# Kernel optimization log

Hardware: AMD Instinct MI355X
Metric: run time of the kernel (lower is better)

## Reference

```python
import jax, jax.numpy as jnp
import numpy as np

NUM_EXPERTS = 8
EMBED_DIM = 512
NUM_LAYERS = 2
LN_EPS = 1e-5


def _all_pairs_hyperedges(E):
    # static 'all_pairs' strategy: one hyperedge per unordered expert pair
    nodes, edges = [], []
    eid = 0
    for i in range(E):
        for j in range(i + 1, E):
            nodes += [i, j]
            edges += [eid, eid]
            eid += 1
    return np.asarray(nodes, np.int32), np.asarray(edges, np.int32)


def setup_inputs() -> dict:
    key = jax.random.key(0)
    ks = jax.random.split(key, 4)
    B, L, E, D = 8, 1024, NUM_EXPERTS, EMBED_DIM
    nodes, edges = _all_pairs_hyperedges(E)
    return {
        "expert_outputs": jax.random.normal(ks[0], (B, L, E, D), jnp.float32),
        # HypergraphConv: lin has bias=False, conv bias is separate
        "hgnn_w": jax.random.normal(ks[1], (NUM_LAYERS, D, D), jnp.float32) * 0.02,
        "hgnn_b": jnp.zeros((NUM_LAYERS, D), jnp.float32),
        # combiner: Linear(D,D) -> GELU -> LayerNorm(D)
        "comb_w": jax.random.normal(ks[2], (D, D), jnp.float32) * 0.02,
        "comb_b": jnp.zeros((D,), jnp.float32),
        "ln_gamma": jnp.ones((D,), jnp.float32),
        "ln_beta": jnp.zeros((D,), jnp.float32),
        "nodes_idx": jnp.asarray(nodes),
        "edges_idx": jnp.asarray(edges),
    }


def _hypergraph_conv(h, W, b, nodes_idx, edges_idx, num_edges, d_inv, b_inv):
    # h: [N, E, D] with N = B*L token-graphs sharing the static hyperedge structure.
    # PyG HypergraphConv (no attention, unit edge weights):
    #   out = D^{-1} H B^{-1} H^T (h @ W^T) + b
    x = jnp.einsum('ned,fd->nef', h, W)  # lin(x), bias=False
    N, E, D = x.shape
    # node -> hyperedge scatter-add, scaled by inverse hyperedge degree B^{-1}
    m = jnp.zeros((N, num_edges, D), x.dtype)
    m = m.at[:, edges_idx].add(x[:, nodes_idx]) * b_inv[None, :, None]
    # hyperedge -> node scatter-add, scaled by inverse node degree D^{-1}
    out = jnp.zeros((N, E, D), x.dtype)
    out = out.at[:, nodes_idx].add(m[:, edges_idx]) * d_inv[None, :, None]
    return out + b


def reference(expert_outputs, hgnn_w, hgnn_b, comb_w, comb_b, ln_gamma, ln_beta, nodes_idx, edges_idx):
    B, L, E, D = expert_outputs.shape
    num_edges = nodes_idx.shape[0] // 2  # all_pairs: exactly 2 nodes per hyperedge
    # degree normalizations (unit hyperedge weights)
    deg = jnp.zeros((E,), expert_outputs.dtype).at[nodes_idx].add(1.0)
    d_inv = jnp.where(deg > 0, 1.0 / deg, 0.0)
    edeg = jnp.zeros((num_edges,), expert_outputs.dtype).at[edges_idx].add(1.0)
    b_inv = jnp.where(edeg > 0, 1.0 / edeg, 0.0)

    h = expert_outputs.reshape(B * L, E, D)
    for l in range(hgnn_w.shape[0]):
        h = _hypergraph_conv(h, hgnn_w[l], hgnn_b[l], nodes_idx, edges_idx, num_edges, d_inv, b_inv)

    pooled = h.reshape(B, L, E, D).mean(axis=2)  # [B, L, D]
    z = jax.nn.gelu(pooled @ comb_w.T + comb_b, approximate=False)  # torch nn.GELU = exact
    mu = jnp.mean(z, axis=-1, keepdims=True)
    var = jnp.var(z, axis=-1, keepdims=True)
    return (z - mu) / jnp.sqrt(var + LN_EPS) * ln_gamma + ln_beta
```

## Files before the change

kernel.cpp:

```cpp
#include <hip/hip_runtime.h>
#include <hip/hip_bf16.h>
#include <math.h>


#define DD 512
#define NTOK 8192

typedef short s16x8 __attribute__((ext_vector_type(8)));
typedef short s16x4 __attribute__((ext_vector_type(4)));
typedef float f32x4 __attribute__((ext_vector_type(4)));

static __device__ __forceinline__ short f2bf(float x) {
  unsigned u = __builtin_bit_cast(unsigned, x);
  unsigned r = (u + 0x7fffu + ((u >> 16) & 1u)) >> 16;
  return (short)r;
}

__global__ __launch_bounds__(256) void pool_kernel(const float* __restrict__ in,
                                                   short* __restrict__ gbf) {
  const int total = NTOK * (DD / 4);
  for (int i = blockIdx.x * blockDim.x + threadIdx.x; i < total;
       i += gridDim.x * blockDim.x) {
    int n = i >> 7;
    int d4 = (i & 127) << 2;
    const float* p = in + (size_t)n * (8 * DD) + d4;
    f32x4 s = {0.f, 0.f, 0.f, 0.f};
#pragma unroll
    for (int e = 0; e < 8; ++e) s += *(const f32x4*)(p + e * DD);
    s *= 0.125f;
    s16x4 o;
    o[0] = f2bf(s[0]); o[1] = f2bf(s[1]); o[2] = f2bf(s[2]); o[3] = f2bf(s[3]);
    *(s16x4*)(gbf + (size_t)n * DD + d4) = o;
  }
}

__global__ __launch_bounds__(256) void cast2_kernel(const float* __restrict__ w2,
                                                    const float* __restrict__ wc,
                                                    short* __restrict__ w2b,
                                                    short* __restrict__ wcb) {
  int i = blockIdx.x * blockDim.x + threadIdx.x;
  const float* src = (i < 65536) ? w2 : wc;
  short* dst = (i < 65536) ? w2b : wcb;
  int j = (i & 65535) << 2;
  f32x4 v = *(const f32x4*)(src + j);
  s16x4 o;
  o[0] = f2bf(v[0]); o[1] = f2bf(v[1]); o[2] = f2bf(v[2]); o[3] = f2bf(v[3]);
  *(s16x4*)(dst + j) = o;
}

__global__ __launch_bounds__(256) void casttr_kernel(const float* __restrict__ w1,
                                                     short* __restrict__ w1t) {
  __shared__ float t[32][33];
  int bx = blockIdx.x & 15, by = blockIdx.x >> 4;
  int tx = threadIdx.x & 31, ty8 = threadIdx.x >> 5;
  int r0 = by * 32, c0 = bx * 32;
#pragma unroll
  for (int j = 0; j < 4; ++j) {
    int r = ty8 * 4 + j;
    t[r][tx] = w1[(size_t)(r0 + r) * DD + c0 + tx];
  }
  __syncthreads();
#pragma unroll
  for (int j = 0; j < 4; ++j) {
    int r = ty8 * 4 + j;
    w1t[(size_t)(c0 + r) * DD + r0 + tx] = f2bf(t[tx][r]);
  }
}

__global__ __launch_bounds__(256) void mv_kernel(const float* __restrict__ M,
                                                 const float* __restrict__ v,
                                                 const float* __restrict__ add,
                                                 float* __restrict__ outv) {
  int w = (blockIdx.x * blockDim.x + threadIdx.x) >> 6;
  int l = threadIdx.x & 63;
  if (w >= DD) return;
  float s = 0.f;
  for (int k = l; k < DD; k += 64) s += M[(size_t)w * DD + k] * v[k];
#pragma unroll
  for (int m = 32; m; m >>= 1) s += __shfl_xor(s, m);
  if (l == 0) outv[w] = s + add[w];
}

__global__ __launch_bounds__(256) void wgemm_kernel(const short* __restrict__ A,
                                                    const short* __restrict__ B,
                                                    short* __restrict__ Out) {
  int w = threadIdx.x >> 6, l = threadIdx.x & 63;
  int lr = l & 15, lg = l >> 4;
  int m0 = (blockIdx.x >> 3) * 64 + w * 16;
  int n0 = (blockIdx.x & 7) * 64;
  f32x4 acc[4] = {};
  const short* ap = A + (size_t)(m0 + lr) * DD + 8 * lg;
  const short* bp = B + (size_t)(n0 + lr) * DD + 8 * lg;
#pragma unroll
  for (int k0 = 0; k0 < DD; k0 += 32) {
    s16x8 a = *(const s16x8*)(ap + k0);
#pragma unroll
    for (int f = 0; f < 4; ++f) {
      s16x8 b = *(const s16x8*)(bp + (size_t)f * 16 * DD + k0);
      acc[f] = __builtin_amdgcn_mfma_f32_16x16x32_bf16(a, b, acc[f], 0, 0, 0);
    }
  }
#pragma unroll
  for (int f = 0; f < 4; ++f)
#pragma unroll
    for (int r = 0; r < 4; ++r)
      Out[(size_t)(m0 + lg * 4 + r) * DD + n0 + f * 16 + lr] = f2bf(acc[f][r]);
}

__global__ __launch_bounds__(256) void main_kernel(
    const short* __restrict__ gbf, const short* __restrict__ wcomb,
    const float* __restrict__ cbias, const float* __restrict__ gamma,
    const float* __restrict__ beta, float* __restrict__ out) {
  __shared__ short As[32 * DD];
  __shared__ float red[32][4][2];
  int tid = threadIdx.x;
  int w = tid >> 6, l = tid & 63;
  int lr = l & 15, lg = l >> 4;
  int m0 = blockIdx.x * 32;

  {
    const char* gs = (const char*)(gbf + (size_t)m0 * DD);
    char* ls = (char*)As;
#pragma unroll
    for (int j = 0; j < 8; ++j) {
      int ci = tid + 256 * j;
      int row = ci >> 6;
      int bo = (ci & 63) << 4;
      s16x8 v = *(const s16x8*)(gs + row * 1024 + bo);
      *(s16x8*)(ls + row * 1024 + (bo ^ ((row & 7) << 4))) = v;
    }
  }
  __syncthreads();

  f32x4 acc[2][8] = {};
  const short* bbase = wcomb + (size_t)(w * 128 + lr) * DD + 8 * lg;
  const char* lsc = (const char*)As;
  for (int k0 = 0; k0 < DD; k0 += 32) {
    int kb = (k0 + 8 * lg) * 2;
    int row0 = lr, row1 = 16 + lr;
    s16x8 a0 = *(const s16x8*)(lsc + row0 * 1024 + (kb ^ ((row0 & 7) << 4)));
    s16x8 a1 = *(const s16x8*)(lsc + row1 * 1024 + (kb ^ ((row1 & 7) << 4)));
#pragma unroll
    for (int f = 0; f < 8; ++f) {
      s16x8 b = *(const s16x8*)(bbase + (size_t)f * 16 * DD + k0);
      acc[0][f] = __builtin_amdgcn_mfma_f32_16x16x32_bf16(a0, b, acc[0][f], 0, 0, 0);
      acc[1][f] = __builtin_amdgcn_mfma_f32_16x16x32_bf16(a1, b, acc[1][f], 0, 0, 0);
    }
  }

  int cbase = w * 128 + lr;
  float s1[2][4] = {}, s2[2][4] = {};
#pragma unroll
  for (int mi = 0; mi < 2; ++mi)
#pragma unroll
    for (int f = 0; f < 8; ++f) {
      float cb = cbias[cbase + f * 16];
#pragma unroll
      for (int r = 0; r < 4; ++r) {
        float x = acc[mi][f][r] + cb;
        float z = 0.5f * x * (1.0f + erff(x * 0.70710678118f));
        acc[mi][f][r] = z;
        s1[mi][r] += z;
        s2[mi][r] += z * z;
      }
    }
#pragma unroll
  for (int m = 1; m < 16; m <<= 1)
#pragma unroll
    for (int mi = 0; mi < 2; ++mi)
#pragma unroll
      for (int r = 0; r < 4; ++r) {
        s1[mi][r] += __shfl_xor(s1[mi][r], m);
        s2[mi][r] += __shfl_xor(s2[mi][r], m);
      }
  if (lr == 0) {
#pragma unroll
    for (int mi = 0; mi < 2; ++mi)
#pragma unroll
      for (int r = 0; r < 4; ++r) {
        int row = mi * 16 + lg * 4 + r;
        red[row][w][0] = s1[mi][r];
        red[row][w][1] = s2[mi][r];
      }
  }
  __syncthreads();
#pragma unroll
  for (int mi = 0; mi < 2; ++mi)
#pragma unroll
    for (int r = 0; r < 4; ++r) {
      int row = mi * 16 + lg * 4 + r;
      float t1 = red[row][0][0] + red[row][1][0] + red[row][2][0] + red[row][3][0];
      float t2 = red[row][0][1] + red[row][1][1] + red[row][2][1] + red[row][3][1];
      float mu = t1 * (1.0f / 512.0f);
      float var = t2 * (1.0f / 512.0f) - mu * mu;
      float rs = rsqrtf(var + 1e-5f);
      float* op = out + (size_t)(m0 + row) * DD;
#pragma unroll
      for (int f = 0; f < 8; ++f) {
        int c = cbase + f * 16;
        op[c] = (acc[mi][f][r] - mu) * rs * gamma[c] + beta[c];
      }
    }
}

extern "C" void kernel_launch(void* const* d_in, const int* in_sizes, int n_in,
                              void* d_out, int out_size, void* d_ws, size_t ws_size,
                              hipStream_t stream) {
  const float* x   = (const float*)d_in[0];
  const float* hw  = (const float*)d_in[1];
  const float* hb  = (const float*)d_in[2];
  const float* cw  = (const float*)d_in[3];
  const float* cb  = (const float*)d_in[4];
  const float* gam = (const float*)d_in[5];
  const float* bet = (const float*)d_in[6];
  float* out = (float*)d_out;

  char* ws = (char*)d_ws;
  short* gbf   = (short*)ws; ws += (size_t)NTOK * DD * 2;
  short* w1t   = (short*)ws; ws += DD * DD * 2;
  short* w2b   = (short*)ws; ws += DD * DD * 2;
  short* wcb   = (short*)ws; ws += DD * DD * 2;
  short* w21t  = (short*)ws; ws += DD * DD * 2;
  short* wcomb = (short*)ws; ws += DD * DD * 2;
  float* tmpv  = (float*)ws; ws += DD * 4;
  float* cbias = (float*)ws; ws += DD * 4;

  const float* W1 = hw;
  const float* W2 = hw + DD * DD;
  const float* b1 = hb;
  const float* b2 = hb + DD;

  pool_kernel<<<2048, 256, 0, stream>>>(x, gbf);
  casttr_kernel<<<256, 256, 0, stream>>>(W1, w1t);
  cast2_kernel<<<512, 256, 0, stream>>>(W2, cw, w2b, wcb);
  mv_kernel<<<128, 256, 0, stream>>>(W2, b1, b2, tmpv);
  mv_kernel<<<128, 256, 0, stream>>>(cw, tmpv, cb, cbias);
  wgemm_kernel<<<64, 256, 0, stream>>>(w1t, w2b, w21t);
  wgemm_kernel<<<64, 256, 0, stream>>>(wcb, w21t, wcomb);
  main_kernel<<<NTOK / 32, 256, 0, stream>>>(gbf, wcomb, cbias, gam, bet, out);
}
```

Before: 280.1 us.

## Fuse pooling into main GEMM kernel and merge weight-prep launches

```diff
diff --git a/kernel.cpp b/kernel.cpp
--- a/kernel.cpp
+++ b/kernel.cpp
@@ -16,63 +16,21 @@
   return (short)r;
 }
 
-__global__ __launch_bounds__(256) void pool_kernel(const float* __restrict__ in,
-                                                   short* __restrict__ gbf) {
-  const int total = NTOK * (DD / 4);
-  for (int i = blockIdx.x * blockDim.x + threadIdx.x; i < total;
-       i += gridDim.x * blockDim.x) {
-    int n = i >> 7;
-    int d4 = (i & 127) << 2;
-    const float* p = in + (size_t)n * (8 * DD) + d4;
-    f32x4 s = {0.f, 0.f, 0.f, 0.f};
-#pragma unroll
-    for (int e = 0; e < 8; ++e) s += *(const f32x4*)(p + e * DD);
-    s *= 0.125f;
-    s16x4 o;
-    o[0] = f2bf(s[0]); o[1] = f2bf(s[1]); o[2] = f2bf(s[2]); o[3] = f2bf(s[3]);
-    *(s16x4*)(gbf + (size_t)n * DD + d4) = o;
-  }
-}
-
-__global__ __launch_bounds__(256) void cast2_kernel(const float* __restrict__ w2,
-                                                    const float* __restrict__ wc,
-                                                    short* __restrict__ w2b,
-                                                    short* __restrict__ wcb) {
-  int i = blockIdx.x * blockDim.x + threadIdx.x;
-  const float* src = (i < 65536) ? w2 : wc;
-  short* dst = (i < 65536) ? w2b : wcb;
-  int j = (i & 65535) << 2;
+static __device__ __forceinline__ void do_cast4(const float* __restrict__ src,
+                                                short* __restrict__ dst, int i) {
+  int j = i << 2;
   f32x4 v = *(const f32x4*)(src + j);
   s16x4 o;
   o[0] = f2bf(v[0]); o[1] = f2bf(v[1]); o[2] = f2bf(v[2]); o[3] = f2bf(v[3]);
   *(s16x4*)(dst + j) = o;
 }
 
-__global__ __launch_bounds__(256) void casttr_kernel(const float* __restrict__ w1,
-                                                     short* __restrict__ w1t) {
-  __shared__ float t[32][33];
-  int bx = blockIdx.x & 15, by = blockIdx.x >> 4;
-  int tx = threadIdx.x & 31, ty8 = threadIdx.x >> 5;
-  int r0 = by * 32, c0 = bx * 32;
-#pragma unroll
-  for (int j = 0; j < 4; ++j) {
-    int r = ty8 * 4 + j;
-    t[r][tx] = w1[(size_t)(r0 + r) * DD + c0 + tx];
-  }
-  __syncthreads();
-#pragma unroll
-  for (int j = 0; j < 4; ++j) {
-    int r = ty8 * 4 + j;
-    w1t[(size_t)(c0 + r) * DD + r0 + tx] = f2bf(t[tx][r]);
-  }
-}
-
-__global__ __launch_bounds__(256) void mv_kernel(const float* __restrict__ M,
-                                                 const float* __restrict__ v,
-                                                 const float* __restrict__ add,
-                                                 float* __restrict__ outv) {
-  int w = (blockIdx.x * blockDim.x + threadIdx.x) >> 6;
-  int l = threadIdx.x & 63;
+static __device__ __forceinline__ void do_mv(const float* __restrict__ M,
+                                             const float* __restrict__ v,
+                                             const float* __restrict__ add,
+                                             float* __restrict__ outv,
+                                             int gtid) {
+  int w = gtid >> 6, l = gtid & 63;
   if (w >= DD) return;
   float s = 0.f;
   for (int k = l; k < DD; k += 64) s += M[(size_t)w * DD + k] * v[k];
@@ -81,13 +39,46 @@
   if (l == 0) outv[w] = s + add[w];
 }
 
-__global__ __launch_bounds__(256) void wgemm_kernel(const short* __restrict__ A,
-                                                    const short* __restrict__ B,
-                                                    short* __restrict__ Out) {
-  int w = threadIdx.x >> 6, l = threadIdx.x & 63;
+__global__ __launch_bounds__(256) void prep1_kernel(
+    const float* __restrict__ w1, const float* __restrict__ w2,
+    const float* __restrict__ wc, const float* __restrict__ b1,
+    const float* __restrict__ b2, short* __restrict__ w1t,
+    short* __restrict__ w2b, short* __restrict__ wcb,
+    float* __restrict__ tmpv) {
+  int b = blockIdx.x, tid = threadIdx.x;
+  if (b < 256) {
+    __shared__ float t[32][33];
+    int bx = b & 15, by = b >> 4;
+    int tx = tid & 31, ty8 = tid >> 5;
+    int r0 = by * 32, c0 = bx * 32;
+#pragma unroll
+    for (int j = 0; j < 4; ++j) {
+      int r = ty8 * 4 + j;
+      t[r][tx] = w1[(size_t)(r0 + r) * DD + c0 + tx];
+    }
+    __syncthreads();
+#pragma unroll
+    for (int j = 0; j < 4; ++j) {
+      int r = ty8 * 4 + j;
+      w1t[(size_t)(c0 + r) * DD + r0 + tx] = f2bf(t[tx][r]);
+    }
+  } else if (b < 768) {
+    int i = (b - 256) * 256 + tid;
+    if (i < 65536) do_cast4(w2, w2b, i);
+    else           do_cast4(wc, wcb, i - 65536);
+  } else {
+    do_mv(w2, b1, b2, tmpv, (b - 768) * 256 + tid);
+  }
+}
+
+static __device__ __forceinline__ void do_wgemm(const short* __restrict__ A,
+                                                const short* __restrict__ B,
+                                                short* __restrict__ Out,
+                                                int b, int tid) {
+  int w = tid >> 6, l = tid & 63;
   int lr = l & 15, lg = l >> 4;
-  int m0 = (blockIdx.x >> 3) * 64 + w * 16;
-  int n0 = (blockIdx.x & 7) * 64;
+  int m0 = (b >> 3) * 64 + w * 16;
+  int n0 = (b & 7) * 64;
   f32x4 acc[4] = {};
   const short* ap = A + (size_t)(m0 + lr) * DD + 8 * lg;
   const short* bp = B + (size_t)(n0 + lr) * DD + 8 * lg;
@@ -96,8 +87,8 @@
     s16x8 a = *(const s16x8*)(ap + k0);
 #pragma unroll
     for (int f = 0; f < 4; ++f) {
-      s16x8 b = *(const s16x8*)(bp + (size_t)f * 16 * DD + k0);
-      acc[f] = __builtin_amdgcn_mfma_f32_16x16x32_bf16(a, b, acc[f], 0, 0, 0);
+      s16x8 bb = *(const s16x8*)(bp + (size_t)f * 16 * DD + k0);
+      acc[f] = __builtin_amdgcn_mfma_f32_16x16x32_bf16(a, bb, acc[f], 0, 0, 0);
     }
   }
 #pragma unroll
@@ -107,100 +98,112 @@
       Out[(size_t)(m0 + lg * 4 + r) * DD + n0 + f * 16 + lr] = f2bf(acc[f][r]);
 }
 
+__global__ __launch_bounds__(256) void prep2_kernel(
+    const short* __restrict__ w1t, const short* __restrict__ w2b,
+    short* __restrict__ w21t, const float* __restrict__ wc,
+    const float* __restrict__ tmpv, const float* __restrict__ cb,
+    float* __restrict__ cbias) {
+  int b = blockIdx.x, tid = threadIdx.x;
+  if (b < 64) do_wgemm(w1t, w2b, w21t, b, tid);
+  else        do_mv(wc, tmpv, cb, cbias, (b - 64) * 256 + tid);
+}
+
+__global__ __launch_bounds__(256) void prep3_kernel(const short* __restrict__ wcb,
+                                                    const short* __restrict__ w21t,
+                                                    short* __restrict__ wcomb) {
+  do_wgemm(wcb, w21t, wcomb, blockIdx.x, threadIdx.x);
+}
+
 __global__ __launch_bounds__(256) void main_kernel(
-    const short* __restrict__ gbf, const short* __restrict__ wcomb,
+    const float* __restrict__ x, const short* __restrict__ wcomb,
     const float* __restrict__ cbias, const float* __restrict__ gamma,
     const float* __restrict__ beta, float* __restrict__ out) {
-  __shared__ short As[32 * DD];
-  __shared__ float red[32][4][2];
+  __shared__ short As[16 * DD];
+  __shared__ float red[16][4][2];
   int tid = threadIdx.x;
   int w = tid >> 6, l = tid & 63;
   int lr = l & 15, lg = l >> 4;
-  int m0 = blockIdx.x * 32;
+  int m0 = blockIdx.x * 16;
 
   {
-    const char* gs = (const char*)(gbf + (size_t)m0 * DD);
+    const float* xb = x + (size_t)m0 * (8 * DD);
     char* ls = (char*)As;
 #pragma unroll
     for (int j = 0; j < 8; ++j) {
-      int ci = tid + 256 * j;
-      int row = ci >> 6;
-      int bo = (ci & 63) << 4;
-      s16x8 v = *(const s16x8*)(gs + row * 1024 + bo);
-      *(s16x8*)(ls + row * 1024 + (bo ^ ((row & 7) << 4))) = v;
+      int i = tid + 256 * j;
+      int n = i >> 7;
+      int d4 = (i & 127) << 2;
+      const float* p = xb + n * (8 * DD) + d4;
+      f32x4 s = {0.f, 0.f, 0.f, 0.f};
+#pragma unroll
+      for (int e = 0; e < 8; ++e) s += *(const f32x4*)(p + e * DD);
+      s *= 0.125f;
+      s16x4 o;
+      o[0] = f2bf(s[0]); o[1] = f2bf(s[1]); o[2] = f2bf(s[2]); o[3] = f2bf(s[3]);
+      int bo = d4 << 1;
+      *(s16x4*)(ls + n * 1024 + (bo ^ ((n & 7) << 4))) = o;
     }
   }
   __syncthreads();
 
-  f32x4 acc[2][8] = {};
+  f32x4 acc[8] = {};
   const short* bbase = wcomb + (size_t)(w * 128 + lr) * DD + 8 * lg;
   const char* lsc = (const char*)As;
   for (int k0 = 0; k0 < DD; k0 += 32) {
     int kb = (k0 + 8 * lg) * 2;
-    int row0 = lr, row1 = 16 + lr;
-    s16x8 a0 = *(const s16x8*)(lsc + row0 * 1024 + (kb ^ ((row0 & 7) << 4)));
-    s16x8 a1 = *(const s16x8*)(lsc + row1 * 1024 + (kb ^ ((row1 & 7) << 4)));
+    s16x8 a = *(const s16x8*)(lsc + lr * 1024 + (kb ^ ((lr & 7) << 4)));
 #pragma unroll
     for (int f = 0; f < 8; ++f) {
       s16x8 b = *(const s16x8*)(bbase + (size_t)f * 16 * DD + k0);
-      acc[0][f] = __builtin_amdgcn_mfma_f32_16x16x32_bf16(a0, b, acc[0][f], 0, 0, 0);
-      acc[1][f] = __builtin_amdgcn_mfma_f32_16x16x32_bf16(a1, b, acc[1][f], 0, 0, 0);
+      acc[f] = __builtin_amdgcn_mfma_f32_16x16x32_bf16(a, b, acc[f], 0, 0, 0);
     }
   }
 
   int cbase = w * 128 + lr;
-  float s1[2][4] = {}, s2[2][4] = {};
-#pragma unroll
-  for (int mi = 0; mi < 2; ++mi)
+  float s1[4] = {}, s2[4] = {};
+#pragma unroll
+  for (int f = 0; f < 8; ++f) {
+    float cb = cbias[cbase + f * 16];
+#pragma unroll
+    for (int r = 0; r < 4; ++r) {
+      float xx = acc[f][r] + cb;
+      float z = 0.5f * xx * (1.0f + erff(xx * 0.70710678118f));
+      acc[f][r] = z;
+      s1[r] += z;
+      s2[r] += z * z;
+    }
+  }
+#pragma unroll
+  for (int m = 1; m < 16; m <<= 1)
+#pragma unroll
+    for (int r = 0; r < 4; ++r) {
+      s1[r] += __shfl_xor(s1[r], m);
+      s2[r] += __shfl_xor(s2[r], m);
+    }
+  if (lr == 0) {
+#pragma unroll
+    for (int r = 0; r < 4; ++r) {
+      int row = lg * 4 + r;
+      red[row][w][0] = s1[r];
+      red[row][w][1] = s2[r];
+    }
+  }
+  __syncthreads();
+#pragma unroll
+  for (int r = 0; r < 4; ++r) {
+    int row = lg * 4 + r;
+    float t1 = red[row][0][0] + red[row][1][0] + red[row][2][0] + red[row][3][0];
+    float t2 = red[row][0][1] + red[row][1][1] + red[row][2][1] + red[row][3][1];
+    float mu = t1 * (1.0f / 512.0f);
+    float var = t2 * (1.0f / 512.0f) - mu * mu;
+    float rs = rsqrtf(var + 1e-5f);
+    float* op = out + (size_t)(m0 + row) * DD;
 #pragma unroll
     for (int f = 0; f < 8; ++f) {
-      float cb = cbias[cbase + f * 16];
-#pragma unroll
-      for (int r = 0; r < 4; ++r) {
-        float x = acc[mi][f][r] + cb;
-        float z = 0.5f * x * (1.0f + erff(x * 0.70710678118f));
-        acc[mi][f][r] = z;
-        s1[mi][r] += z;
-        s2[mi][r] += z * z;
-      }
-    }
-#pragma unroll
-  for (int m = 1; m < 16; m <<= 1)
-#pragma unroll
-    for (int mi = 0; mi < 2; ++mi)
-#pragma unroll
-      for (int r = 0; r < 4; ++r) {
-        s1[mi][r] += __shfl_xor(s1[mi][r], m);
-        s2[mi][r] += __shfl_xor(s2[mi][r], m);
-      }
-  if (lr == 0) {
-#pragma unroll
-    for (int mi = 0; mi < 2; ++mi)
-#pragma unroll
-      for (int r = 0; r < 4; ++r) {
-        int row = mi * 16 + lg * 4 + r;
-        red[row][w][0] = s1[mi][r];
-        red[row][w][1] = s2[mi][r];
-      }
-  }
-  __syncthreads();
-#pragma unroll
-  for (int mi = 0; mi < 2; ++mi)
-#pragma unroll
-    for (int r = 0; r < 4; ++r) {
-      int row = mi * 16 + lg * 4 + r;
-      float t1 = red[row][0][0] + red[row][1][0] + red[row][2][0] + red[row][3][0];
-      float t2 = red[row][0][1] + red[row][1][1] + red[row][2][1] + red[row][3][1];
-      float mu = t1 * (1.0f / 512.0f);
-      float var = t2 * (1.0f / 512.0f) - mu * mu;
-      float rs = rsqrtf(var + 1e-5f);
-      float* op = out + (size_t)(m0 + row) * DD;
-#pragma unroll
-      for (int f = 0; f < 8; ++f) {
-        int c = cbase + f * 16;
-        op[c] = (acc[mi][f][r] - mu) * rs * gamma[c] + beta[c];
-      }
-    }
+      int c = cbase + f * 16;
+      op[c] = (acc[f][r] - mu) * rs * gamma[c] + beta[c];
+    }
+  }
 }
 
 extern "C" void kernel_launch(void* const* d_in, const int* in_sizes, int n_in,
@@ -216,7 +219,6 @@
   float* out = (float*)d_out;
 
   char* ws = (char*)d_ws;
-  short* gbf   = (short*)ws; ws += (size_t)NTOK * DD * 2;
   short* w1t   = (short*)ws; ws += DD * DD * 2;
   short* w2b   = (short*)ws; ws += DD * DD * 2;
   short* wcb   = (short*)ws; ws += DD * DD * 2;
@@ -230,12 +232,8 @@
   const float* b1 = hb;
   const float* b2 = hb + DD;
 
-  pool_kernel<<<2048, 256, 0, stream>>>(x, gbf);
-  casttr_kernel<<<256, 256, 0, stream>>>(W1, w1t);
-  cast2_kernel<<<512, 256, 0, stream>>>(W2, cw, w2b, wcb);
-  mv_kernel<<<128, 256, 0, stream>>>(W2, b1, b2, tmpv);
-  mv_kernel<<<128, 256, 0, stream>>>(cw, tmpv, cb, cbias);
-  wgemm_kernel<<<64, 256, 0, stream>>>(w1t, w2b, w21t);
-  wgemm_kernel<<<64, 256, 0, stream>>>(wcb, w21t, wcomb);
-  main_kernel<<<NTOK / 32, 256, 0, stream>>>(gbf, wcomb, cbias, gam, bet, out);
-}
+  prep1_kernel<<<896, 256, 0, stream>>>(W1, W2, cw, b1, b2, w1t, w2b, wcb, tmpv);
+  prep2_kernel<<<192, 256, 0, stream>>>(w1t, w2b, w21t, cw, tmpv, cb, cbias);
+  prep3_kernel<<<64, 256, 0, stream>>>(wcb, w21t, wcomb);
+  main_kernel<<<NTOK / 16, 256, 0, stream>>>(x, wcomb, cbias, gam, bet, out);
+}
```

Result: faster. 261.0 us (-6.8%).
